# Performance work log

Measured on AMD Instinct MI355X. Metric: run time of the kernel, lower is better.

## Reference

```python
import jax, jax.numpy as jnp
import numpy as np

E = 1024  # embedding_dim
D = 1024  # output_dim

def setup_inputs() -> dict:
    key = jax.random.key(0)
    k_x, k_q, k_k, k_v = jax.random.split(key, 4)
    embeddings = jax.random.normal(k_x, (4, 2048, E), dtype=jnp.float32)
    scale = 1.0 / np.sqrt(E)
    Wq = jax.random.normal(k_q, (E, D), dtype=jnp.float32) * scale
    Wk = jax.random.normal(k_k, (E, D), dtype=jnp.float32) * scale
    Wv = jax.random.normal(k_v, (E, D), dtype=jnp.float32) * scale
    return {"embeddings": embeddings, "Wq": Wq, "Wk": Wk, "Wv": Wv}

def reference(embeddings, Wq, Wk, Wv):
    # QKV projections (no bias, qkv_bias=False)
    q = jnp.einsum('bse,ed->bsd', embeddings, Wq)
    k = jnp.einsum('bse,ed->bsd', embeddings, Wk)
    v = jnp.einsum('bse,ed->bsd', embeddings, Wv)
    n = embeddings.shape[1]
    scores = jnp.einsum('bqd,bkd->bqk', q, k)  # [B, S, S]
    causal = jnp.tril(jnp.ones((n, n), dtype=bool))  # mask upper triangle (diag=1)
    scores = jnp.where(causal, scores, -jnp.inf)
    scale = jnp.asarray(k.shape[-1], scores.dtype) ** 0.5
    weights = jax.nn.softmax(scores / scale, axis=-1)
    # dropout p=0.0 -> identity
    context = jnp.einsum('bqk,bkd->bqd', weights, v)
    return context
```

## Files before the change

### kernel.cpp

```cpp
#include <hip/hip_runtime.h>

typedef unsigned short u16;
typedef __attribute__((ext_vector_type(8))) short short8;
typedef __attribute__((ext_vector_type(4))) float f32x4;
typedef __attribute__((ext_vector_type(4))) unsigned short u16x4;
typedef __attribute__((ext_vector_type(4))) float float4v;

__device__ __forceinline__ u16 f2bf(float f) {
  union { float f; unsigned u; } v; v.f = f;
  unsigned r = v.u + 0x7FFFu + ((v.u >> 16) & 1u);
  return (u16)(r >> 16);
}

__device__ __forceinline__ void gload16(const void* g, void* l) {
  __builtin_amdgcn_global_load_lds(
      (const __attribute__((address_space(1))) unsigned int*)g,
      (__attribute__((address_space(3))) unsigned int*)l, 16, 0, 0);
}


__global__ __launch_bounds__(256) void kconv_x(const float* __restrict__ X,
                                               u16* __restrict__ Xb) {
  size_t i = ((size_t)blockIdx.x * 256 + threadIdx.x) * 4;
  float4v v = *(const float4v*)(X + i);
  u16x4 o;
  o.x = f2bf(v.x); o.y = f2bf(v.y); o.z = f2bf(v.z); o.w = f2bf(v.w);
  *(u16x4*)(Xb + i) = o;
}

__global__ __launch_bounds__(256) void kconv_wt(const float* __restrict__ Wq,
                                                const float* __restrict__ Wk,
                                                const float* __restrict__ Wv,
                                                u16* __restrict__ Wt) {
  __shared__ float tile[32][33];
  const float* W = blockIdx.z == 0 ? Wq : (blockIdx.z == 1 ? Wk : Wv);
  u16* O = Wt + (size_t)blockIdx.z * 1024 * 1024;
  int tx = threadIdx.x, ty = threadIdx.y;
  int n0 = blockIdx.x * 32, k0 = blockIdx.y * 32;
#pragma unroll
  for (int r = 0; r < 32; r += 8)
    tile[ty + r][tx] = W[(size_t)(k0 + ty + r) * 1024 + n0 + tx];
  __syncthreads();
#pragma unroll
  for (int r = 0; r < 32; r += 8)
    O[(size_t)(n0 + ty + r) * 1024 + k0 + tx] = f2bf(tile[tx][ty + r]);
}

__device__ __forceinline__ void gemm_inner(const u16* __restrict__ A,
                                           const u16* __restrict__ B,
                                           int lda, int ldb,
                                           int rowBase, int colBase, int kIters,
                                           u16* As, u16* Bs, f32x4 acc[4][4]) {
  const int t = threadIdx.x;
  const int wid = t >> 6, lane = t & 63;
  const int wm = wid >> 1, wn = wid & 1;
  const int lrow = lane & 15, kseg = (lane >> 4) * 8;
  const u16* ga = A + (size_t)(rowBase + (t >> 2)) * lda + ((t & 3) * 8);
  const u16* gb = B + (size_t)(colBase + (t >> 2)) * ldb + ((t & 3) * 8);
  u16* la0 = As + wid * 512;
  u16* la1 = As + 2048 + wid * 512;
  u16* lb0 = Bs + wid * 512;
  u16* lb1 = Bs + 2048 + wid * 512;
  const size_t a64 = (size_t)64 * lda, b64 = (size_t)64 * ldb;

  for (int kt = 0; kt < kIters; ++kt) {
    const int k0 = kt * 32;
    gload16(ga + k0, la0);
    gload16(ga + a64 + k0, la1);
    gload16(gb + k0, lb0);
    gload16(gb + b64 + k0, lb1);
    __syncthreads();
    short8 a[4], b[4];
#pragma unroll
    for (int mi = 0; mi < 4; mi++)
      a[mi] = *(const short8*)(As + (wm * 64 + mi * 16 + lrow) * 32 + kseg);
#pragma unroll
    for (int ni = 0; ni < 4; ni++)
      b[ni] = *(const short8*)(Bs + (wn * 64 + ni * 16 + lrow) * 32 + kseg);
#pragma unroll
    for (int mi = 0; mi < 4; mi++)
#pragma unroll
      for (int ni = 0; ni < 4; ni++)
        acc[mi][ni] = __builtin_amdgcn_mfma_f32_16x16x32_bf16(
            a[mi], b[ni], acc[mi][ni], 0, 0, 0);
    __syncthreads();
  }
}

__global__ __launch_bounds__(256, 3) void kqkv(const u16* __restrict__ Xb,
                                               const u16* __restrict__ Wt,
                                               u16* __restrict__ Qb,
                                               u16* __restrict__ Kb,
                                               u16* __restrict__ Vt) {
  __shared__ __align__(16) u16 As[4096];
  __shared__ __align__(16) u16 Bs[4096];
  const f32x4 z4 = {0.f, 0.f, 0.f, 0.f};
  f32x4 acc[4][4];
#pragma unroll
  for (int i = 0; i < 4; i++)
#pragma unroll
    for (int j = 0; j < 4; j++) acc[i][j] = z4;

  const int l = blockIdx.x;
  const int xcd = l & 7, idx = l >> 3;
  const int cz = idx >> 3, rloc = idx & 7;
  const int rowTile = xcd * 8 + rloc;
  const int z = cz >> 3, colTile = cz & 7;

  const int rowBase = rowTile * 128, colBase = colTile * 128;
  const u16* Bt = Wt + (size_t)z * 1024 * 1024;
  gemm_inner(Xb, Bt, 1024, 1024, rowBase, colBase, 32, As, Bs, acc);

  const int t = threadIdx.x, wid = t >> 6, lane = t & 63;
  const int wm = wid >> 1, wn = wid & 1;
  const int r0 = rowBase + wm * 64 + ((lane >> 4) * 4);
  const int c0 = colBase + wn * 64 + (lane & 15);
  if (z < 2) {
    u16* O = z ? Kb : Qb;
#pragma unroll
    for (int mi = 0; mi < 4; mi++) {
      int r = r0 + mi * 16;
#pragma unroll
      for (int ni = 0; ni < 4; ni++) {
        int c = c0 + ni * 16;
#pragma unroll
        for (int j = 0; j < 4; j++)
          O[(size_t)(r + j) * 1024 + c] = f2bf(acc[mi][ni][j]);
      }
    }
  } else {
#pragma unroll
    for (int mi = 0; mi < 4; mi++) {
      int s0 = r0 + mi * 16;
      int bb = s0 >> 11, sl = s0 & 2047;
#pragma unroll
      for (int ni = 0; ni < 4; ni++) {
        int d = c0 + ni * 16;
        u16x4 pk;
        pk.x = f2bf(acc[mi][ni][0]);
        pk.y = f2bf(acc[mi][ni][1]);
        pk.z = f2bf(acc[mi][ni][2]);
        pk.w = f2bf(acc[mi][ni][3]);
        *(u16x4*)(Vt + ((size_t)bb * 1024 + d) * 2048 + sl) = pk;
      }
    }
  }
}

__global__ __launch_bounds__(256, 3) void kscores(const u16* __restrict__ Q,
                                                  const u16* __restrict__ K,
                                                  float* __restrict__ Sc) {
  const int x = blockIdx.x, b = blockIdx.y;
  const int xcd = x & 7, idx = x >> 3;
  const int tid = xcd * 17 + idx;
  int tr = (int)((sqrtf(8.f * tid + 1.f) - 1.f) * 0.5f);
  while ((tr + 1) * (tr + 2) / 2 <= tid) ++tr;
  while (tr * (tr + 1) / 2 > tid) --tr;
  const int tc = tid - tr * (tr + 1) / 2;

  __shared__ __align__(16) u16 As[4096];
  __shared__ __align__(16) u16 Bs[4096];
  const f32x4 z4 = {0.f, 0.f, 0.f, 0.f};
  f32x4 acc[4][4];
#pragma unroll
  for (int i = 0; i < 4; i++)
#pragma unroll
    for (int j = 0; j < 4; j++) acc[i][j] = z4;

  const u16* Qp = Q + (size_t)b * 2048 * 1024;
  const u16* Kp = K + (size_t)b * 2048 * 1024;
  gemm_inner(Qp, Kp, 1024, 1024, tr * 128, tc * 128, 32, As, Bs, acc);

  float* S = Sc + (size_t)b * 2048 * 2048;
  const int t = threadIdx.x, wid = t >> 6, lane = t & 63;
  const int wm = wid >> 1, wn = wid & 1;
  const int r0 = tr * 128 + wm * 64 + ((lane >> 4) * 4);
  const int c0 = tc * 128 + wn * 64 + (lane & 15);
#pragma unroll
  for (int mi = 0; mi < 4; mi++) {
    int r = r0 + mi * 16;
#pragma unroll
    for (int ni = 0; ni < 4; ni++) {
      int c = c0 + ni * 16;
#pragma unroll
      for (int j = 0; j < 4; j++)
        S[(size_t)(r + j) * 2048 + c] = acc[mi][ni][j] * 0.03125f;
    }
  }
}

__global__ __launch_bounds__(256) void ksoftmax(const float* __restrict__ Sc,
                                                u16* __restrict__ P) {
  const int i = blockIdx.x, b = blockIdx.y;
  const int nv = i + 1;
  const int nceil = ((i >> 7) + 1) << 7;
  const float* S = Sc + ((size_t)b * 2048 + i) * 2048;
  u16* Pr = P + ((size_t)b * 2048 + i) * 2048;
  __shared__ float srow[2048];
  __shared__ float red[4];
  const int t = threadIdx.x, lane = t & 63, wid = t >> 6;

  float lm = -3.0e38f;
  for (int j = t; j < nv; j += 256) {
    float v = S[j];
    srow[j] = v;
    lm = fmaxf(lm, v);
  }
#pragma unroll
  for (int o = 32; o > 0; o >>= 1) lm = fmaxf(lm, __shfl_down(lm, o));
  if (lane == 0) red[wid] = lm;
  __syncthreads();
  const float m = fmaxf(fmaxf(red[0], red[1]), fmaxf(red[2], red[3]));

  float ls = 0.f;
  for (int j = t; j < nv; j += 256) {
    float e = __expf(srow[j] - m);
    srow[j] = e;
    ls += e;
  }
#pragma unroll
  for (int o = 32; o > 0; o >>= 1) ls += __shfl_down(ls, o);
  __syncthreads();
  if (lane == 0) red[wid] = ls;
  __syncthreads();
  const float inv = 1.f / (red[0] + red[1] + red[2] + red[3]);

  for (int j = t; j < nv; j += 256) Pr[j] = f2bf(srow[j] * inv);
  for (int j = nv + t; j < nceil; j += 256) Pr[j] = 0;
}

__global__ __launch_bounds__(256, 3) void kpv(const u16* __restrict__ P,
                                              const u16* __restrict__ Vt,
                                              float* __restrict__ Out) {
  const int x = blockIdx.x, b = blockIdx.y;
  const int xcd = x & 7, idx = x >> 3;
  const int tr = (idx < 8) ? xcd : (15 - xcd);
  const int col = idx & 7;

  __shared__ __align__(16) u16 As[4096];
  __shared__ __align__(16) u16 Bs[4096];
  const f32x4 z4 = {0.f, 0.f, 0.f, 0.f};
  f32x4 acc[4][4];
#pragma unroll
  for (int i = 0; i < 4; i++)
#pragma unroll
    for (int j = 0; j < 4; j++) acc[i][j] = z4;

  const u16* Pp = P + (size_t)b * 2048 * 2048;
  const u16* Vp = Vt + (size_t)b * 1024 * 2048;
  gemm_inner(Pp, Vp, 2048, 2048, tr * 128, col * 128, (tr + 1) * 4, As, Bs, acc);

  float* Ob = Out + (size_t)b * 2048 * 1024;
  const int t = threadIdx.x, wid = t >> 6, lane = t & 63;
  const int wm = wid >> 1, wn = wid & 1;
  const int r0 = tr * 128 + wm * 64 + ((lane >> 4) * 4);
  const int c0 = col * 128 + wn * 64 + (lane & 15);
#pragma unroll
  for (int mi = 0; mi < 4; mi++) {
    int r = r0 + mi * 16;
#pragma unroll
    for (int ni = 0; ni < 4; ni++) {
      int c = c0 + ni * 16;
#pragma unroll
      for (int j = 0; j < 4; j++)
        Ob[(size_t)(r + j) * 1024 + c] = acc[mi][ni][j];
    }
  }
}

extern "C" void kernel_launch(void* const* d_in, const int* in_sizes, int n_in,
                              void* d_out, int out_size, void* d_ws,
                              size_t ws_size, hipStream_t stream) {
  const float* X = (const float*)d_in[0];
  const float* Wq = (const float*)d_in[1];
  const float* Wk = (const float*)d_in[2];
  const float* Wv = (const float*)d_in[3];
  float* Out = (float*)d_out;

  char* ws = (char*)d_ws;
  u16* Xb = (u16*)(ws);
  u16* Wt = (u16*)(ws + 16777216);
  u16* Qb = (u16*)(ws + 23068672);
  u16* Kb = (u16*)(ws + 39845888);
  u16* Vt = (u16*)(ws + 56623104);
  float* Sc = (float*)(ws + 73400320);
  u16* P = (u16*)(ws + 140509184);

  kconv_x<<<8192, 256, 0, stream>>>(X, Xb);
  kconv_wt<<<dim3(32, 32, 3), dim3(32, 8), 0, stream>>>(Wq, Wk, Wv, Wt);
  kqkv<<<1536, 256, 0, stream>>>(Xb, Wt, Qb, Kb, Vt);
  kscores<<<dim3(136, 4), 256, 0, stream>>>(Qb, Kb, Sc);
  ksoftmax<<<dim3(2048, 4), 256, 0, stream>>>(Sc, P);
  kpv<<<dim3(128, 4), 256, 0, stream>>>(P, Vt, Out);
}
```

Before: 172.4 us.

## Double GEMM K-tile to 64 with XOR-swizzled LDS and merge conversion kernels

Each GEMM loop iteration now stages a 128x64 K-slice instead of 128x32 into LDS. That halves the number of barrier pairs per tile. An XOR swizzle on the LDS layout is meant to avoid bank conflicts on the wider rows. The two conversion kernels for X and the weights are merged into one launch to save a kernel launch. LDS use per block doubles, to 32KB, which may reduce occupancy.

```diff
diff --git a/kernel.cpp b/kernel.cpp
--- a/kernel.cpp
+++ b/kernel.cpp
@@ -18,71 +18,88 @@
       (__attribute__((address_space(3))) unsigned int*)l, 16, 0, 0);
 }
 
-
-__global__ __launch_bounds__(256) void kconv_x(const float* __restrict__ X,
-                                               u16* __restrict__ Xb) {
-  size_t i = ((size_t)blockIdx.x * 256 + threadIdx.x) * 4;
-  float4v v = *(const float4v*)(X + i);
-  u16x4 o;
-  o.x = f2bf(v.x); o.y = f2bf(v.y); o.z = f2bf(v.z); o.w = f2bf(v.w);
-  *(u16x4*)(Xb + i) = o;
-}
-
-__global__ __launch_bounds__(256) void kconv_wt(const float* __restrict__ Wq,
-                                                const float* __restrict__ Wk,
-                                                const float* __restrict__ Wv,
-                                                u16* __restrict__ Wt) {
+__global__ __launch_bounds__(256) void kconv(const float* __restrict__ X,
+                                             const float* __restrict__ Wq,
+                                             const float* __restrict__ Wk,
+                                             const float* __restrict__ Wv,
+                                             u16* __restrict__ Xb,
+                                             u16* __restrict__ Wt) {
   __shared__ float tile[32][33];
-  const float* W = blockIdx.z == 0 ? Wq : (blockIdx.z == 1 ? Wk : Wv);
-  u16* O = Wt + (size_t)blockIdx.z * 1024 * 1024;
-  int tx = threadIdx.x, ty = threadIdx.y;
-  int n0 = blockIdx.x * 32, k0 = blockIdx.y * 32;
-#pragma unroll
-  for (int r = 0; r < 32; r += 8)
-    tile[ty + r][tx] = W[(size_t)(k0 + ty + r) * 1024 + n0 + tx];
-  __syncthreads();
-#pragma unroll
-  for (int r = 0; r < 32; r += 8)
-    O[(size_t)(n0 + ty + r) * 1024 + k0 + tx] = f2bf(tile[tx][ty + r]);
-}
-
-__device__ __forceinline__ void gemm_inner(const u16* __restrict__ A,
-                                           const u16* __restrict__ B,
-                                           int lda, int ldb,
-                                           int rowBase, int colBase, int kIters,
-                                           u16* As, u16* Bs, f32x4 acc[4][4]) {
+  const int bx = blockIdx.x;
+  if (bx < 8192) {
+    size_t i = ((size_t)bx * 256 + threadIdx.x) * 4;
+    float4v v = *(const float4v*)(X + i);
+    u16x4 o;
+    o.x = f2bf(v.x); o.y = f2bf(v.y); o.z = f2bf(v.z); o.w = f2bf(v.w);
+    *(u16x4*)(Xb + i) = o;
+  } else {
+    const int l = bx - 8192;
+    const int z = l >> 10;
+    const int rem = l & 1023;
+    const int n0 = (rem & 31) * 32, k0 = (rem >> 5) * 32;
+    const float* W = z == 0 ? Wq : (z == 1 ? Wk : Wv);
+    u16* O = Wt + (size_t)z * 1024 * 1024;
+    const int tx = threadIdx.x & 31, ty = threadIdx.x >> 5;
+#pragma unroll
+    for (int r = 0; r < 32; r += 8)
+      tile[ty + r][tx] = W[(size_t)(k0 + ty + r) * 1024 + n0 + tx];
+    __syncthreads();
+#pragma unroll
+    for (int r = 0; r < 32; r += 8)
+      O[(size_t)(n0 + ty + r) * 1024 + k0 + tx] = f2bf(tile[tx][ty + r]);
+  }
+}
+
+__device__ __forceinline__ void stage64(const u16* __restrict__ pan, int ld,
+                                        int k0, u16* dst, int t) {
+  const int rb = t >> 3;
+  const int sw = ((t & 7) ^ (rb & 7)) * 8;
+  const int ds = (t & 7) * 8;
+#pragma unroll
+  for (int j = 0; j < 4; ++j) {
+    const int row = j * 32 + rb;
+    gload16(pan + (size_t)row * ld + k0 + sw, dst + row * 64 + ds);
+  }
+}
+
+__device__ __forceinline__ void gemm64(const u16* __restrict__ A,
+                                       const u16* __restrict__ B,
+                                       int lda, int ldb,
+                                       int rowBase, int colBase, int kIters,
+                                       u16* As, u16* Bs, f32x4 acc[4][4]) {
   const int t = threadIdx.x;
   const int wid = t >> 6, lane = t & 63;
   const int wm = wid >> 1, wn = wid & 1;
-  const int lrow = lane & 15, kseg = (lane >> 4) * 8;
-  const u16* ga = A + (size_t)(rowBase + (t >> 2)) * lda + ((t & 3) * 8);
-  const u16* gb = B + (size_t)(colBase + (t >> 2)) * ldb + ((t & 3) * 8);
-  u16* la0 = As + wid * 512;
-  u16* la1 = As + 2048 + wid * 512;
-  u16* lb0 = Bs + wid * 512;
-  u16* lb1 = Bs + 2048 + wid * 512;
-  const size_t a64 = (size_t)64 * lda, b64 = (size_t)64 * ldb;
+  const int l15 = lane & 15;
+  const int sw = l15 & 7;
+  const int sl = lane >> 4;
+  const int s0 = ((sl    ) ^ sw) * 8;
+  const int s1 = ((sl + 4) ^ sw) * 8;
+  const u16* ga = A + (size_t)rowBase * lda;
+  const u16* gb = B + (size_t)colBase * ldb;
 
   for (int kt = 0; kt < kIters; ++kt) {
-    const int k0 = kt * 32;
-    gload16(ga + k0, la0);
-    gload16(ga + a64 + k0, la1);
-    gload16(gb + k0, lb0);
-    gload16(gb + b64 + k0, lb1);
+    const int k0 = kt * 64;
+    stage64(ga, lda, k0, As, t);
+    stage64(gb, ldb, k0, Bs, t);
     __syncthreads();
-    short8 a[4], b[4];
-#pragma unroll
-    for (int mi = 0; mi < 4; mi++)
-      a[mi] = *(const short8*)(As + (wm * 64 + mi * 16 + lrow) * 32 + kseg);
-#pragma unroll
-    for (int ni = 0; ni < 4; ni++)
-      b[ni] = *(const short8*)(Bs + (wn * 64 + ni * 16 + lrow) * 32 + kseg);
-#pragma unroll
-    for (int mi = 0; mi < 4; mi++)
+#pragma unroll
+    for (int h = 0; h < 2; ++h) {
+      const int so = h ? s1 : s0;
+      short8 a[4], b[4];
+#pragma unroll
+      for (int mi = 0; mi < 4; mi++)
+        a[mi] = *(const short8*)(As + (wm * 64 + mi * 16 + l15) * 64 + so);
 #pragma unroll
       for (int ni = 0; ni < 4; ni++)
-        acc[mi][ni] = __builtin_amdgcn_mfma_f32_16x16x32_bf16(
-            a[mi], b[ni], acc[mi][ni], 0, 0, 0);
+        b[ni] = *(const short8*)(Bs + (wn * 64 + ni * 16 + l15) * 64 + so);
+#pragma unroll
+      for (int mi = 0; mi < 4; mi++)
+#pragma unroll
+        for (int ni = 0; ni < 4; ni++)
+          acc[mi][ni] = __builtin_amdgcn_mfma_f32_16x16x32_bf16(
+              a[mi], b[ni], acc[mi][ni], 0, 0, 0);
+    }
     __syncthreads();
   }
 }
@@ -92,8 +109,8 @@
                                                u16* __restrict__ Qb,
                                                u16* __restrict__ Kb,
                                                u16* __restrict__ Vt) {
-  __shared__ __align__(16) u16 As[4096];
-  __shared__ __align__(16) u16 Bs[4096];
+  __shared__ __align__(16) u16 As[128 * 64];
+  __shared__ __align__(16) u16 Bs[128 * 64];
   const f32x4 z4 = {0.f, 0.f, 0.f, 0.f};
   f32x4 acc[4][4];
 #pragma unroll
@@ -109,7 +126,7 @@
 
   const int rowBase = rowTile * 128, colBase = colTile * 128;
   const u16* Bt = Wt + (size_t)z * 1024 * 1024;
-  gemm_inner(Xb, Bt, 1024, 1024, rowBase, colBase, 32, As, Bs, acc);
+  gemm64(Xb, Bt, 1024, 1024, rowBase, colBase, 16, As, Bs, acc);
 
   const int t = threadIdx.x, wid = t >> 6, lane = t & 63;
   const int wm = wid >> 1, wn = wid & 1;
@@ -131,8 +148,8 @@
   } else {
 #pragma unroll
     for (int mi = 0; mi < 4; mi++) {
-      int s0 = r0 + mi * 16;
-      int bb = s0 >> 11, sl = s0 & 2047;
+      int s0r = r0 + mi * 16;
+      int bb = s0r >> 11, sl = s0r & 2047;
 #pragma unroll
       for (int ni = 0; ni < 4; ni++) {
         int d = c0 + ni * 16;
@@ -158,8 +175,8 @@
   while (tr * (tr + 1) / 2 > tid) --tr;
   const int tc = tid - tr * (tr + 1) / 2;
 
-  __shared__ __align__(16) u16 As[4096];
-  __shared__ __align__(16) u16 Bs[4096];
+  __shared__ __align__(16) u16 As[128 * 64];
+  __shared__ __align__(16) u16 Bs[128 * 64];
   const f32x4 z4 = {0.f, 0.f, 0.f, 0.f};
   f32x4 acc[4][4];
 #pragma unroll
@@ -169,7 +186,7 @@
 
   const u16* Qp = Q + (size_t)b * 2048 * 1024;
   const u16* Kp = K + (size_t)b * 2048 * 1024;
-  gemm_inner(Qp, Kp, 1024, 1024, tr * 128, tc * 128, 32, As, Bs, acc);
+  gemm64(Qp, Kp, 1024, 1024, tr * 128, tc * 128, 16, As, Bs, acc);
 
   float* S = Sc + (size_t)b * 2048 * 2048;
   const int t = threadIdx.x, wid = t >> 6, lane = t & 63;
@@ -237,8 +254,8 @@
   const int tr = (idx < 8) ? xcd : (15 - xcd);
   const int col = idx & 7;
 
-  __shared__ __align__(16) u16 As[4096];
-  __shared__ __align__(16) u16 Bs[4096];
+  __shared__ __align__(16) u16 As[128 * 64];
+  __shared__ __align__(16) u16 Bs[128 * 64];
   const f32x4 z4 = {0.f, 0.f, 0.f, 0.f};
   f32x4 acc[4][4];
 #pragma unroll
@@ -248,7 +265,7 @@
 
   const u16* Pp = P + (size_t)b * 2048 * 2048;
   const u16* Vp = Vt + (size_t)b * 1024 * 2048;
-  gemm_inner(Pp, Vp, 2048, 2048, tr * 128, col * 128, (tr + 1) * 4, As, Bs, acc);
+  gemm64(Pp, Vp, 2048, 2048, tr * 128, col * 128, (tr + 1) * 2, As, Bs, acc);
 
   float* Ob = Out + (size_t)b * 2048 * 1024;
   const int t = threadIdx.x, wid = t >> 6, lane = t & 63;
@@ -286,8 +303,7 @@
   float* Sc = (float*)(ws + 73400320);
   u16* P = (u16*)(ws + 140509184);
 
-  kconv_x<<<8192, 256, 0, stream>>>(X, Xb);
-  kconv_wt<<<dim3(32, 32, 3), dim3(32, 8), 0, stream>>>(Wq, Wk, Wv, Wt);
+  kconv<<<11264, 256, 0, stream>>>(X, Wq, Wk, Wv, Xb, Wt);
   kqkv<<<1536, 256, 0, stream>>>(Xb, Wt, Qb, Kb, Vt);
   kscores<<<dim3(136, 4), 256, 0, stream>>>(Qb, Kb, Sc);
   ksoftmax<<<dim3(2048, 4), 256, 0, stream>>>(Sc, P);
```

Measured after the change: 147.7 us. 1.17x faster.
